# Kernel optimization log

Measured on AMD Instinct MI355X. Metric: run time of the kernel, lower is better.

## Reference

```python
import jax, jax.numpy as jnp
import numpy as np

N = 100000   # nodes
E = 3200000  # edges per graph
DP, DA, DF, H, C = 3, 11, 32, 4, 8  # d_p, d_a, d_feat, heads, per-head dim
NEG_SLOPE = 0.2


def gat_conv(x, edge_index, W, att_src, att_dst, bias):
    """PyG GATConv with concat heads and default add_self_loops=True.
    x: [N, DF]; edge_index: [2, E] (row0=src, row1=dst); W: [DF, H*C];
    att_src/att_dst: [H, C]; bias: [H*C]. Returns [N, H*C]."""
    n = x.shape[0]
    loops = jnp.arange(n, dtype=edge_index.dtype)
    src = jnp.concatenate([edge_index[0], loops])
    dst = jnp.concatenate([edge_index[1], loops])
    h = (x @ W).reshape(n, H, C)                       # [N,H,C]
    a_s = jnp.sum(h * att_src[None], axis=-1)          # [N,H]
    a_d = jnp.sum(h * att_dst[None], axis=-1)          # [N,H]
    e = jax.nn.leaky_relu(a_s[src] + a_d[dst], NEG_SLOPE)  # [Etot,H]
    m = jax.ops.segment_max(e, dst, num_segments=n)        # stable softmax per dst
    ex = jnp.exp(e - m[dst])
    den = jax.ops.segment_sum(ex, dst, num_segments=n)
    alpha = ex / den[dst]                               # [Etot,H]
    out = jax.ops.segment_sum(h[src] * alpha[..., None], dst, num_segments=n)
    return out.reshape(n, H * C) + bias


def setup_inputs() -> dict:
    key = jax.random.key(0)
    ks = jax.random.split(key, 32)
    p = lambda k, shp: (jax.random.normal(k, shp, dtype=jnp.float32) * 0.1)
    inp = {
        "F_p_raw": jax.random.normal(ks[0], (N, DP), dtype=jnp.float32),
        "F_a_raw": jax.random.normal(ks[1], (N, DA), dtype=jnp.float32),
        "edge_index_s": jax.random.randint(ks[2], (2, E), 0, N),
        "edge_index_p": jax.random.randint(ks[3], (2, E), 0, N),
        "edge_index_a": jax.random.randint(ks[4], (2, E), 0, N),
        # align linears
        "Wp": p(ks[5], (DP, DF)), "bp": p(ks[6], (DF,)),
        "Wa": p(ks[7], (DA, DF)), "ba": p(ks[8], (DF,)),
        "Ws": p(ks[9], (DP + DA, DF)), "bs": p(ks[10], (DF,)),
        # GAT params per graph
        "Wg_s": p(ks[11], (DF, H * C)), "asrc_s": p(ks[12], (H, C)), "adst_s": p(ks[13], (H, C)), "bg_s": p(ks[14], (H * C,)),
        "Wg_p": p(ks[15], (DF, H * C)), "asrc_p": p(ks[16], (H, C)), "adst_p": p(ks[17], (H, C)), "bg_p": p(ks[18], (H * C,)),
        "Wg_a": p(ks[19], (DF, H * C)), "asrc_a": p(ks[20], (H, C)), "adst_a": p(ks[21], (H, C)), "bg_a": p(ks[22], (H * C,)),
        # fuse MLP
        "W1": p(ks[23], (3 * DF, DF)), "b1": p(ks[24], (DF,)),
        "W2": p(ks[25], (DF, DF)), "b2": p(ks[26], (DF,)),
    }
    return inp


def reference(F_p_raw, F_a_raw, edge_index_s, edge_index_p, edge_index_a,
              Wp, bp, Wa, ba, Ws, bs,
              Wg_s, asrc_s, adst_s, bg_s,
              Wg_p, asrc_p, adst_p, bg_p,
              Wg_a, asrc_a, adst_a, bg_a,
              W1, b1, W2, b2):
    f_s = jnp.concatenate([F_p_raw, F_a_raw], axis=-1) @ Ws + bs
    f_p = F_p_raw @ Wp + bp
    f_a = F_a_raw @ Wa + ba
    h_s = jax.nn.elu(gat_conv(f_s, edge_index_s, Wg_s, asrc_s, adst_s, bg_s))
    h_p = jax.nn.elu(gat_conv(f_p, edge_index_p, Wg_p, asrc_p, adst_p, bg_p))
    h_a = jax.nn.elu(gat_conv(f_a, edge_index_a, Wg_a, asrc_a, adst_a, bg_a))
    h = jnp.concatenate([h_s, h_p, h_a], axis=-1)
    h = jax.nn.relu(h @ W1 + b1)
    return h @ W2 + b2
```

## Files before the change

### kernel.cpp

```cpp
#include <hip/hip_runtime.h>
#include <hip/hip_bf16.h>
#include <stdint.h>

typedef __hip_bfloat16 bf16;

__device__ __forceinline__ float b2f(bf16 v){ return __bfloat162float(v); }

__device__ __forceinline__ uint16_t f2b(float x){
  uint32_t u = __float_as_uint(x);
  return (uint16_t)((u + 0x7FFFu + ((u >> 16) & 1u)) >> 16);
}

#define DSTS_PER_BKT 128
#define BKT_SHIFT 7
#define CHUNKE 8192
#define CAP 8192
#define PPT 32
#define BIN_IT 32
#define MAXB 1024
#define NBLKMAX 512
#define ROWS_PER_WAVE (DSTS_PER_BKT / 4)

struct CvtTab {
  const void* src[24];
  int n[24];
  int off[24];
};

__global__ __launch_bounds__(256) void k_detect(const void* __restrict__ sample,
                                                int* __restrict__ flag)
{
  __shared__ int bad;
  if (threadIdx.x == 0) bad = 0;
  __syncthreads();
  const unsigned short* u = (const unsigned short*)sample;
  int lbad = 0;
  for (int k = threadIdx.x; k < 1024; k += 256) {
    unsigned short b = u[k];
    unsigned e = (b >> 7) & 0xFFu;
    if (e >= 141u || (e <= 90u && (b & 0x7FFFu) != 0)) lbad = 1;
  }
  if (lbad) atomicOr(&bad, 1);
  __syncthreads();
  if (threadIdx.x == 0) flag[0] = (bad == 0) ? 1 : 0;
}

__global__ __launch_bounds__(256) void k_convert(CvtTab tab, const int* __restrict__ flag,
                                                 float* __restrict__ dst, int total)
{
  const bool isb = (*flag) != 0;
  for (int t = blockIdx.x * 256 + threadIdx.x; t < total; t += gridDim.x * 256) {
    int a = 0;
    while (a < 23 && t >= tab.off[a] + tab.n[a]) ++a;
    int j = t - tab.off[a];
    float v = isb ? b2f(((const bf16*)tab.src[a])[j])
                  : ((const float*)tab.src[a])[j];
    dst[t] = v;
  }
}

__global__ __launch_bounds__(256) void k_node(
  const float* __restrict__ cFp, const float* __restrict__ cFa,
  const float* __restrict__ cWp, const float* __restrict__ cbp,
  const float* __restrict__ cWa, const float* __restrict__ cba,
  const float* __restrict__ cWs, const float* __restrict__ cbs,
  const float* __restrict__ cWg0, const float* __restrict__ cAs0, const float* __restrict__ cAd0,
  const float* __restrict__ cWg1, const float* __restrict__ cAs1, const float* __restrict__ cAd1,
  const float* __restrict__ cWg2, const float* __restrict__ cAs2, const float* __restrict__ cAd2,
  uint32_t* __restrict__ hgb, uint16_t* __restrict__ asb, float* __restrict__ a_d,
  float* __restrict__ den, float* __restrict__ agg, int N)
{
  __shared__ float sWs[14*32];
  __shared__ float sWp[3*32];
  __shared__ float sWa[11*32];
  __shared__ float sb[3][32];
  __shared__ float sWg[3][32*32];
  __shared__ float sA[3][2][32];
  const int tid = threadIdx.x;
  for (int t = tid; t < 14*32; t += 256) sWs[t] = cWs[t];
  for (int t = tid; t < 3*32;  t += 256) sWp[t] = cWp[t];
  for (int t = tid; t < 11*32; t += 256) sWa[t] = cWa[t];
  if (tid < 32) {
    sb[0][tid] = cbs[tid]; sb[1][tid] = cbp[tid]; sb[2][tid] = cba[tid];
    sA[0][0][tid] = cAs0[tid]; sA[0][1][tid] = cAd0[tid];
    sA[1][0][tid] = cAs1[tid]; sA[1][1][tid] = cAd1[tid];
    sA[2][0][tid] = cAs2[tid]; sA[2][1][tid] = cAd2[tid];
  }
  for (int t = tid; t < 32*32; t += 256) {
    sWg[0][t] = cWg0[t]; sWg[1][t] = cWg1[t]; sWg[2][t] = cWg2[t];
  }
  __syncthreads();

  const int i = blockIdx.x * 256 + tid;
  if (i >= N) return;

  float xp[3], xa[11];
  #pragma unroll
  for (int k = 0; k < 3; ++k)  xp[k] = cFp[i*3 + k];
  #pragma unroll
  for (int k = 0; k < 11; ++k) xa[k] = cFa[i*11 + k];

  for (int g = 0; g < 3; ++g) {
    float f[32];
    if (g == 0) {
      #pragma unroll
      for (int j = 0; j < 32; ++j) {
        float acc = sb[0][j];
        #pragma unroll
        for (int k = 0; k < 3; ++k)  acc += xp[k] * sWs[k*32 + j];
        #pragma unroll
        for (int k = 0; k < 11; ++k) acc += xa[k] * sWs[(3+k)*32 + j];
        f[j] = acc;
      }
    } else if (g == 1) {
      #pragma unroll
      for (int j = 0; j < 32; ++j) {
        float acc = sb[1][j];
        #pragma unroll
        for (int k = 0; k < 3; ++k) acc += xp[k] * sWp[k*32 + j];
        f[j] = acc;
      }
    } else {
      #pragma unroll
      for (int j = 0; j < 32; ++j) {
        float acc = sb[2][j];
        #pragma unroll
        for (int k = 0; k < 11; ++k) acc += xa[k] * sWa[k*32 + j];
        f[j] = acc;
      }
    }

    const float* Wg = sWg[g];
    float hv[32];
    #pragma unroll
    for (int j = 0; j < 32; ++j) {
      float acc = 0.f;
      #pragma unroll
      for (int k = 0; k < 32; ++k) acc += f[k] * Wg[k*32 + j];
      hv[j] = acc;
    }

    float asv[4], adv[4], exv[4];
    #pragma unroll
    for (int h = 0; h < 4; ++h) {
      float s0 = 0.f, s1 = 0.f;
      #pragma unroll
      for (int c = 0; c < 8; ++c) {
        s0 += hv[h*8 + c] * sA[g][0][h*8 + c];
        s1 += hv[h*8 + c] * sA[g][1][h*8 + c];
      }
      asv[h] = s0; adv[h] = s1;
      float e = s0 + s1;
      e = e > 0.f ? e : 0.2f * e;
      exv[h] = __expf(e);
    }

    const size_t row = (size_t)g * N + i;
    uint32_t* hp = hgb + row * 16;
    #pragma unroll
    for (int q = 0; q < 4; ++q) {
      uint4 u;
      u.x = (uint32_t)f2b(hv[q*8+0]) | ((uint32_t)f2b(hv[q*8+1]) << 16);
      u.y = (uint32_t)f2b(hv[q*8+2]) | ((uint32_t)f2b(hv[q*8+3]) << 16);
      u.z = (uint32_t)f2b(hv[q*8+4]) | ((uint32_t)f2b(hv[q*8+5]) << 16);
      u.w = (uint32_t)f2b(hv[q*8+6]) | ((uint32_t)f2b(hv[q*8+7]) << 16);
      *(uint4*)(hp + q*4) = u;
    }
    *(ushort4*)(asb + row * 4) =
        make_ushort4(f2b(asv[0]), f2b(asv[1]), f2b(asv[2]), f2b(asv[3]));

    float4* agp = (float4*)(agg + row * 32);
    #pragma unroll
    for (int q = 0; q < 8; ++q) {
      float ex = exv[q >> 1];
      agp[q] = make_float4(ex*hv[q*4+0], ex*hv[q*4+1], ex*hv[q*4+2], ex*hv[q*4+3]);
    }
    *(float4*)(a_d + row*4) = make_float4(adv[0], adv[1], adv[2], adv[3]);
    *(float4*)(den + row*4) = make_float4(exv[0], exv[1], exv[2], exv[3]);
  }
}

__global__ __launch_bounds__(256) void k_bin2(
  const int* __restrict__ ei0, const int* __restrict__ ei1, const int* __restrict__ ei2,
  int* __restrict__ dir, int* __restrict__ bins, int NBPG, int NBLK, int E)
{
  const int g = blockIdx.y;
  const int* __restrict__ ei = (g == 0) ? ei0 : (g == 1 ? ei1 : ei2);
  __shared__ int sp[CHUNKE];
  __shared__ int hist[MAXB];
  __shared__ int soff[MAXB + 1];
  __shared__ int s[256];
  const int tid = threadIdx.x;
  const int blk = blockIdx.x;
  const int base = blk * CHUNKE;
  const int m = min(CHUNKE, E - base);

  for (int t = tid; t < NBPG; t += 256) hist[t] = 0;
  __syncthreads();

  int pk[BIN_IT];
  #pragma unroll
  for (int k = 0; k < BIN_IT; ++k) {
    int idx = base + k * 256 + tid;
    if (idx < E) {
      int d = ei[E + idx];
      int b = d >> BKT_SHIFT;
      int loc = atomicAdd(&hist[b], 1);
      pk[k] = (b << 20) | (loc << 7) | (d & (DSTS_PER_BKT - 1));
    } else pk[k] = -1;
  }
  __syncthreads();

  {
    const int sb = tid * 4;
    int v[4]; int sum = 0;
    #pragma unroll
    for (int j = 0; j < 4; ++j) {
      int i = sb + j; int x = (i < NBPG) ? hist[i] : 0; v[j] = x; sum += x;
    }
    s[tid] = sum;
    __syncthreads();
    for (int d = 1; d < 256; d <<= 1) {
      int t = (tid >= d) ? s[tid - d] : 0;
      __syncthreads();
      s[tid] += t;
      __syncthreads();
    }
    int run = s[tid] - sum;
    #pragma unroll
    for (int j = 0; j < 4; ++j) {
      int i = sb + j;
      if (i < NBPG) { soff[i] = run; run += v[j]; }
    }
    if (tid == 255) soff[NBPG] = s[255];
  }
  __syncthreads();

  for (int t = tid; t <= NBPG; t += 256)
    dir[((size_t)(g * (NBPG + 1) + t)) * NBLK + blk] = soff[t];

  #pragma unroll
  for (int k = 0; k < BIN_IT; ++k) {
    int p = pk[k];
    if (p >= 0) {
      int idx = base + k * 256 + tid;
      int src = ei[idx];
      int b   = p >> 20;
      int loc = (p >> 7) & 0x1FFF;
      int dl  = p & (DSTS_PER_BKT - 1);
      sp[soff[b] + loc] = (dl << 17) | src;
    }
  }
  __syncthreads();

  const size_t ob = ((size_t)(g * NBLK + blk)) << 13;
  for (int i = tid; i < m; i += 256) bins[ob + i] = sp[i];
}

__global__ __launch_bounds__(256, 4) void k_vgather(
  const int* __restrict__ dir, const int* __restrict__ bins,
  const uint32_t* __restrict__ hgb, const uint16_t* __restrict__ asb,
  const float* __restrict__ a_d,
  float* __restrict__ den, float* __restrict__ agg, int NBPG, int NBLK, int N)
{
  __shared__ int sorted[CAP];
  __shared__ int runbase[NBLKMAX];
  __shared__ int pbase[NBLKMAX + 1];
  __shared__ int soff[DSTS_PER_BKT + 1];
  __shared__ int scnt[DSTS_PER_BKT];
  __shared__ int sscan[DSTS_PER_BKT];
  __shared__ int s[256];
  __shared__ int schunk;
  const int g = blockIdx.y, b = blockIdx.x, tid = threadIdx.x;
  const int wave = tid >> 6;
  const int lane = tid & 63;
  const int sub  = lane >> 4;
  const int l16  = lane & 15;
  const int h    = l16 >> 2;
  const int grp16 = tid >> 4;
  const int ln16  = tid & 15;
  const size_t gbase = (size_t)g * N;
  const int dst0 = b * DSTS_PER_BKT;

  const int* d0 = dir + ((size_t)(g * (NBPG + 1) + b)) * NBLK;
  const int* d1 = d0 + NBLK;
  for (int t = tid; t < NBLK; t += 256) {
    int r0 = d0[t], r1 = d1[t];
    runbase[t] = ((g * NBLK + t) << 13) + r0;
    pbase[t] = r1 - r0;
  }
  __syncthreads();
  {
    int v0 = (2*tid     < NBLK) ? pbase[2*tid]     : 0;
    int v1 = (2*tid + 1 < NBLK) ? pbase[2*tid + 1] : 0;
    __syncthreads();
    int sum = v0 + v1; s[tid] = sum;
    __syncthreads();
    for (int d = 1; d < 256; d <<= 1) {
      int t = (tid >= d) ? s[tid - d] : 0;
      __syncthreads();
      s[tid] += t;
      __syncthreads();
    }
    int run = s[tid] - sum;
    if (2*tid     <= NBLK) pbase[2*tid]     = run;
    if (2*tid + 1 <= NBLK) pbase[2*tid + 1] = run + v0;
  }
  __syncthreads();
  const int ntot = pbase[NBLK];

  int rlo = 0;
  while (rlo < NBLK) {
    if (tid == 0) {
      if (rlo == 0 && ntot <= CAP) schunk = NBLK;
      else {
        int lim = pbase[rlo] + CAP;
        int hi = rlo + 1;
        while (hi < NBLK && pbase[hi + 1] <= lim) ++hi;
        schunk = hi;
      }
    }
    if (tid < DSTS_PER_BKT) scnt[tid] = 0;
    __syncthreads();
    const int rhi = schunk;
    const int pb0 = pbase[rlo];
    const int m = pbase[rhi] - pb0;

    for (int rr = rlo + grp16; rr < rhi; rr += 16) {
      const int l = pbase[rr + 1] - pbase[rr];
      const int gbb = runbase[rr];
      const int ldst = pbase[rr] - pb0;
      for (int i = ln16; i < l; i += 16) {
        int p = bins[gbb + i];
        sorted[ldst + i] = p;
        atomicAdd(&scnt[(p >> 17) & (DSTS_PER_BKT - 1)], 1);
      }
    }
    __syncthreads();
    if (tid < DSTS_PER_BKT) sscan[tid] = scnt[tid];
    __syncthreads();
    for (int d = 1; d < DSTS_PER_BKT; d <<= 1) {
      int t = 0;
      if (tid < DSTS_PER_BKT && tid >= d) t = sscan[tid - d];
      __syncthreads();
      if (tid < DSTS_PER_BKT) sscan[tid] += t;
      __syncthreads();
    }
    if (tid < DSTS_PER_BKT) {
      int ex = sscan[tid] - scnt[tid];
      soff[tid] = ex;
      scnt[tid] = ex;
    }
    if (tid == 0) soff[DSTS_PER_BKT] = m;
    __syncthreads();
    int pv[PPT];
    #pragma unroll
    for (int k = 0; k < PPT; ++k) {
      int i = k * 256 + tid;
      pv[k] = (i < m) ? sorted[i] : -1;
    }
    __syncthreads();
    #pragma unroll
    for (int k = 0; k < PPT; ++k) {
      int p = pv[k];
      if (p >= 0) {
        int pos = atomicAdd(&scnt[(p >> 17) & (DSTS_PER_BKT - 1)], 1);
        sorted[pos] = p & 0x1FFFF;
      }
    }
    __syncthreads();

    const int rbeg = wave * ROWS_PER_WAVE;
    for (int rl = rbeg; rl < rbeg + ROWS_PER_WAVE; ++rl) {
      const int dst = dst0 + rl;
      if (dst >= N) break;
      const int cs = soff[rl], ce = soff[rl + 1];
      const size_t row = gbase + dst;
      const float ad = a_d[row * 4 + h];
      float ax = 0.f, ay = 0.f, w = 0.f;
      for (int c = cs + sub; c < ce; c += 16) {
        const int i0 = c        < ce ? sorted[c]      : -1;
        const int i1 = (c + 4)  < ce ? sorted[c + 4]  : -1;
        const int i2 = (c + 8)  < ce ? sorted[c + 8]  : -1;
        const int i3 = (c + 12) < ce ? sorted[c + 12] : -1;
        const int p0 = i0 < 0 ? 0 : i0;
        const int p1 = i1 < 0 ? 0 : i1;
        const int p2 = i2 < 0 ? 0 : i2;
        const int p3 = i3 < 0 ? 0 : i3;
        const uint32_t u0 = hgb[(gbase + p0) * 16 + l16];
        const uint32_t u1 = hgb[(gbase + p1) * 16 + l16];
        const uint32_t u2 = hgb[(gbase + p2) * 16 + l16];
        const uint32_t u3 = hgb[(gbase + p3) * 16 + l16];
        const uint16_t t0 = asb[(gbase + p0) * 4 + h];
        const uint16_t t1 = asb[(gbase + p1) * 4 + h];
        const uint16_t t2 = asb[(gbase + p2) * 4 + h];
        const uint16_t t3 = asb[(gbase + p3) * 4 + h];
        float e0 = __uint_as_float((uint32_t)t0 << 16) + ad; e0 = e0 > 0.f ? e0 : 0.2f * e0;
        float e1 = __uint_as_float((uint32_t)t1 << 16) + ad; e1 = e1 > 0.f ? e1 : 0.2f * e1;
        float e2 = __uint_as_float((uint32_t)t2 << 16) + ad; e2 = e2 > 0.f ? e2 : 0.2f * e2;
        float e3 = __uint_as_float((uint32_t)t3 << 16) + ad; e3 = e3 > 0.f ? e3 : 0.2f * e3;
        const float w0 = i0 >= 0 ? __expf(e0) : 0.f;
        const float w1 = i1 >= 0 ? __expf(e1) : 0.f;
        const float w2 = i2 >= 0 ? __expf(e2) : 0.f;
        const float w3 = i3 >= 0 ? __expf(e3) : 0.f;
        ax += w0 * __uint_as_float(u0 << 16);
        ay += w0 * __uint_as_float(u0 & 0xFFFF0000u);
        ax += w1 * __uint_as_float(u1 << 16);
        ay += w1 * __uint_as_float(u1 & 0xFFFF0000u);
        ax += w2 * __uint_as_float(u2 << 16);
        ay += w2 * __uint_as_float(u2 & 0xFFFF0000u);
        ax += w3 * __uint_as_float(u3 << 16);
        ay += w3 * __uint_as_float(u3 & 0xFFFF0000u);
        w += w0 + w1 + w2 + w3;
      }
      ax += __shfl_xor(ax, 16); ay += __shfl_xor(ay, 16); w += __shfl_xor(w, 16);
      ax += __shfl_xor(ax, 32); ay += __shfl_xor(ay, 32); w += __shfl_xor(w, 32);
      if (sub == 0) {
        float2* ap = (float2*)(agg + row * 32) + l16;
        float2 sv = *ap;
        sv.x += ax; sv.y += ay;
        *ap = sv;
        if ((l16 & 3) == 0) den[row * 4 + h] += w;
      }
    }
    __syncthreads();
    rlo = rhi;
  }
}

__global__ __launch_bounds__(256) void k_final(
  const float* __restrict__ den, const float* __restrict__ agg,
  const float* __restrict__ cbg0, const float* __restrict__ cbg1, const float* __restrict__ cbg2,
  const float* __restrict__ cW1, const float* __restrict__ cb1,
  const float* __restrict__ cW2, const float* __restrict__ cb2,
  const int* __restrict__ flag, void* __restrict__ out, int N)
{
  __shared__ float sW1[96*32];
  __shared__ float sW2[32*32];
  __shared__ float sb1[32], sb2[32], sbg[3][32];
  const int tid = threadIdx.x;
  for (int t = tid; t < 96*32; t += 256) sW1[t] = cW1[t];
  for (int t = tid; t < 32*32; t += 256) sW2[t] = cW2[t];
  if (tid < 32) {
    sb1[tid] = cb1[tid]; sb2[tid] = cb2[tid];
    sbg[0][tid] = cbg0[tid]; sbg[1][tid] = cbg1[tid]; sbg[2][tid] = cbg2[tid];
  }
  __syncthreads();

  const int i = blockIdx.x * 256 + tid;
  if (i >= N) return;

  float h96[96];
  #pragma unroll
  for (int g = 0; g < 3; ++g) {
    const size_t row = (size_t)g * N + i;
    float4 d4 = *(const float4*)(den + row * 4);
    float invs[4] = {1.f/d4.x, 1.f/d4.y, 1.f/d4.z, 1.f/d4.w};
    const float4* av = (const float4*)(agg + row * 32);
    #pragma unroll
    for (int q = 0; q < 8; ++q) {
      float4 a4 = av[q];
      float iv = invs[q >> 1];
      float vals[4] = {a4.x, a4.y, a4.z, a4.w};
      #pragma unroll
      for (int k = 0; k < 4; ++k) {
        float v = vals[k] * iv + sbg[g][q*4 + k];
        v = v > 0.f ? v : (__expf(v) - 1.f);
        h96[g*32 + q*4 + k] = v;
      }
    }
  }

  float h1[32];
  #pragma unroll
  for (int j = 0; j < 32; ++j) {
    float acc = sb1[j];
    #pragma unroll
    for (int k = 0; k < 96; ++k) acc += h96[k] * sW1[k*32 + j];
    h1[j] = acc > 0.f ? acc : 0.f;
  }

  const bool isb = (*flag) != 0;
  #pragma unroll
  for (int j = 0; j < 32; ++j) {
    float acc = sb2[j];
    #pragma unroll
    for (int k = 0; k < 32; ++k) acc += h1[k] * sW2[k*32 + j];
    if (isb) ((bf16*)out)[(size_t)i*32 + j] = __float2bfloat16(acc);
    else     ((float*)out)[(size_t)i*32 + j] = acc;
  }
}

extern "C" void kernel_launch(void* const* d_in, const int* in_sizes, int n_in,
                              void* d_out, int out_size, void* d_ws, size_t ws_size,
                              hipStream_t stream)
{
  const int N = in_sizes[0] / 3;
  const int E = in_sizes[2] / 2;
  const int NBPG = (N + DSTS_PER_BKT - 1) / DSTS_PER_BKT;
  const int NBLK = (E + CHUNKE - 1) / CHUNKE;

  float* ws  = (float*)d_ws;
  int* flag  = (int*)d_ws;
  float* cvt = ws + 64;

  static const int order[24] = {1, 0,
    5, 6, 7, 8, 9, 10,
    11, 12, 13, 14,
    15, 16, 17, 18,
    19, 20, 21, 22,
    23, 24, 25, 26};
  CvtTab tab;
  int off0 = 0;
  for (int a = 0; a < 24; ++a) {
    tab.src[a] = d_in[order[a]];
    tab.n[a]   = in_sizes[order[a]];
    tab.off[a] = off0;
    off0 += tab.n[a];
  }
  const int total = off0;

  float* P[24];
  for (int a = 0; a < 24; ++a) P[a] = cvt + tab.off[a];
  float *cFa = P[0],  *cFp = P[1];
  float *cWp = P[2],  *cbp = P[3],  *cWa = P[4],  *cba = P[5],  *cWs = P[6], *cbs = P[7];
  float *cWg0 = P[8],  *cAs0 = P[9],  *cAd0 = P[10], *cbg0 = P[11];
  float *cWg1 = P[12], *cAs1 = P[13], *cAd1 = P[14], *cbg1 = P[15];
  float *cWg2 = P[16], *cAs2 = P[17], *cAd2 = P[18], *cbg2 = P[19];
  float *cW1 = P[20], *cb1 = P[21], *cW2 = P[22], *cb2 = P[23];

  int pad = (4 - (total & 3)) & 3;
  float* big = cvt + total + pad;
  const size_t n3 = (size_t)3 * N;
  float* agg  = big;
  float* a_d  = agg + n3 * 32;
  float* den  = a_d + n3 * 4;
  uint32_t* hgb = (uint32_t*)(den + n3 * 4);
  uint16_t* asb = (uint16_t*)(hgb + n3 * 16);
  int* dir  = (int*)(asb + n3 * 4);
  int* bins = dir + (size_t)3 * (NBPG + 1) * NBLK;

  k_detect<<<1, 256, 0, stream>>>(d_in[1], flag);
  k_convert<<<2048, 256, 0, stream>>>(tab, flag, cvt, total);
  k_node<<<(N + 255) / 256, 256, 0, stream>>>(
      cFp, cFa, cWp, cbp, cWa, cba, cWs, cbs,
      cWg0, cAs0, cAd0, cWg1, cAs1, cAd1, cWg2, cAs2, cAd2,
      hgb, asb, a_d, den, agg, N);

  dim3 gbk((unsigned)NBLK, 3, 1);
  k_bin2<<<gbk, 256, 0, stream>>>(
      (const int*)d_in[2], (const int*)d_in[3], (const int*)d_in[4],
      dir, bins, NBPG, NBLK, E);

  dim3 gg((unsigned)NBPG, 3, 1);
  k_vgather<<<gg, 256, 0, stream>>>(dir, bins, hgb, asb, a_d, den, agg, NBPG, NBLK, N);

  k_final<<<(N + 255) / 256, 256, 0, stream>>>(
      den, agg, cbg0, cbg1, cbg2, cW1, cb1, cW2, cb2, flag, d_out, N);
}
```

Measured before the change: 432.8 us.

## Drop separate conversion kernel and gather bins with flat binary-searched indexing

```diff
diff --git a/kernel.cpp b/kernel.cpp
--- a/kernel.cpp
+++ b/kernel.cpp
@@ -9,6 +9,10 @@
 __device__ __forceinline__ uint16_t f2b(float x){
   uint32_t u = __float_as_uint(x);
   return (uint16_t)((u + 0x7FFFu + ((u >> 16) & 1u)) >> 16);
+}
+
+__device__ __forceinline__ float loadf(const void* p, int j, bool isb){
+  return isb ? b2f(((const bf16*)p)[j]) : ((const float*)p)[j];
 }
 
 #define DSTS_PER_BKT 128
@@ -21,12 +25,6 @@
 #define NBLKMAX 512
 #define ROWS_PER_WAVE (DSTS_PER_BKT / 4)
 
-struct CvtTab {
-  const void* src[24];
-  int n[24];
-  int off[24];
-};
-
 __global__ __launch_bounds__(256) void k_detect(const void* __restrict__ sample,
                                                 int* __restrict__ flag)
 {
@@ -45,28 +43,15 @@
   if (threadIdx.x == 0) flag[0] = (bad == 0) ? 1 : 0;
 }
 
-__global__ __launch_bounds__(256) void k_convert(CvtTab tab, const int* __restrict__ flag,
-                                                 float* __restrict__ dst, int total)
-{
-  const bool isb = (*flag) != 0;
-  for (int t = blockIdx.x * 256 + threadIdx.x; t < total; t += gridDim.x * 256) {
-    int a = 0;
-    while (a < 23 && t >= tab.off[a] + tab.n[a]) ++a;
-    int j = t - tab.off[a];
-    float v = isb ? b2f(((const bf16*)tab.src[a])[j])
-                  : ((const float*)tab.src[a])[j];
-    dst[t] = v;
-  }
-}
-
 __global__ __launch_bounds__(256) void k_node(
-  const float* __restrict__ cFp, const float* __restrict__ cFa,
-  const float* __restrict__ cWp, const float* __restrict__ cbp,
-  const float* __restrict__ cWa, const float* __restrict__ cba,
-  const float* __restrict__ cWs, const float* __restrict__ cbs,
-  const float* __restrict__ cWg0, const float* __restrict__ cAs0, const float* __restrict__ cAd0,
-  const float* __restrict__ cWg1, const float* __restrict__ cAs1, const float* __restrict__ cAd1,
-  const float* __restrict__ cWg2, const float* __restrict__ cAs2, const float* __restrict__ cAd2,
+  const void* __restrict__ rFp, const void* __restrict__ rFa,
+  const void* __restrict__ rWp, const void* __restrict__ rbp,
+  const void* __restrict__ rWa, const void* __restrict__ rba,
+  const void* __restrict__ rWs, const void* __restrict__ rbs,
+  const void* __restrict__ rWg0, const void* __restrict__ rAs0, const void* __restrict__ rAd0,
+  const void* __restrict__ rWg1, const void* __restrict__ rAs1, const void* __restrict__ rAd1,
+  const void* __restrict__ rWg2, const void* __restrict__ rAs2, const void* __restrict__ rAd2,
+  const int* __restrict__ flag,
   uint32_t* __restrict__ hgb, uint16_t* __restrict__ asb, float* __restrict__ a_d,
   float* __restrict__ den, float* __restrict__ agg, int N)
 {
@@ -77,17 +62,22 @@
   __shared__ float sWg[3][32*32];
   __shared__ float sA[3][2][32];
   const int tid = threadIdx.x;
-  for (int t = tid; t < 14*32; t += 256) sWs[t] = cWs[t];
-  for (int t = tid; t < 3*32;  t += 256) sWp[t] = cWp[t];
-  for (int t = tid; t < 11*32; t += 256) sWa[t] = cWa[t];
+  const bool isb = (*flag) != 0;
+  for (int t = tid; t < 14*32; t += 256) sWs[t] = loadf(rWs, t, isb);
+  for (int t = tid; t < 3*32;  t += 256) sWp[t] = loadf(rWp, t, isb);
+  for (int t = tid; t < 11*32; t += 256) sWa[t] = loadf(rWa, t, isb);
   if (tid < 32) {
-    sb[0][tid] = cbs[tid]; sb[1][tid] = cbp[tid]; sb[2][tid] = cba[tid];
-    sA[0][0][tid] = cAs0[tid]; sA[0][1][tid] = cAd0[tid];
-    sA[1][0][tid] = cAs1[tid]; sA[1][1][tid] = cAd1[tid];
-    sA[2][0][tid] = cAs2[tid]; sA[2][1][tid] = cAd2[tid];
+    sb[0][tid] = loadf(rbs, tid, isb);
+    sb[1][tid] = loadf(rbp, tid, isb);
+    sb[2][tid] = loadf(rba, tid, isb);
+    sA[0][0][tid] = loadf(rAs0, tid, isb); sA[0][1][tid] = loadf(rAd0, tid, isb);
+    sA[1][0][tid] = loadf(rAs1, tid, isb); sA[1][1][tid] = loadf(rAd1, tid, isb);
+    sA[2][0][tid] = loadf(rAs2, tid, isb); sA[2][1][tid] = loadf(rAd2, tid, isb);
   }
   for (int t = tid; t < 32*32; t += 256) {
-    sWg[0][t] = cWg0[t]; sWg[1][t] = cWg1[t]; sWg[2][t] = cWg2[t];
+    sWg[0][t] = loadf(rWg0, t, isb);
+    sWg[1][t] = loadf(rWg1, t, isb);
+    sWg[2][t] = loadf(rWg2, t, isb);
   }
   __syncthreads();
 
@@ -96,9 +86,9 @@
 
   float xp[3], xa[11];
   #pragma unroll
-  for (int k = 0; k < 3; ++k)  xp[k] = cFp[i*3 + k];
-  #pragma unroll
-  for (int k = 0; k < 11; ++k) xa[k] = cFa[i*11 + k];
+  for (int k = 0; k < 3; ++k)  xp[k] = loadf(rFp, i*3 + k, isb);
+  #pragma unroll
+  for (int k = 0; k < 11; ++k) xa[k] = loadf(rFa, i*11 + k, isb);
 
   for (int g = 0; g < 3; ++g) {
     float f[32];
@@ -277,8 +267,6 @@
   const int sub  = lane >> 4;
   const int l16  = lane & 15;
   const int h    = l16 >> 2;
-  const int grp16 = tid >> 4;
-  const int ln16  = tid & 15;
   const size_t gbase = (size_t)g * N;
   const int dst0 = b * DSTS_PER_BKT;
 
@@ -326,13 +314,18 @@
     const int pb0 = pbase[rlo];
     const int m = pbase[rhi] - pb0;
 
-    for (int rr = rlo + grp16; rr < rhi; rr += 16) {
-      const int l = pbase[rr + 1] - pbase[rr];
-      const int gbb = runbase[rr];
-      const int ldst = pbase[rr] - pb0;
-      for (int i = ln16; i < l; i += 16) {
-        int p = bins[gbb + i];
-        sorted[ldst + i] = p;
+    #pragma unroll 4
+    for (int k = 0; k < PPT; ++k) {
+      const int j = k * 256 + tid;
+      if (j < m) {
+        const int j0 = pb0 + j;
+        int lo = rlo, hi = rhi;
+        while (hi - lo > 1) {
+          int mid = (lo + hi) >> 1;
+          if (pbase[mid] <= j0) lo = mid; else hi = mid;
+        }
+        int p = bins[runbase[lo] + (j0 - pbase[lo])];
+        sorted[j] = p;
         atomicAdd(&scnt[(p >> 17) & (DSTS_PER_BKT - 1)], 1);
       }
     }
@@ -430,20 +423,23 @@
 
 __global__ __launch_bounds__(256) void k_final(
   const float* __restrict__ den, const float* __restrict__ agg,
-  const float* __restrict__ cbg0, const float* __restrict__ cbg1, const float* __restrict__ cbg2,
-  const float* __restrict__ cW1, const float* __restrict__ cb1,
-  const float* __restrict__ cW2, const float* __restrict__ cb2,
+  const void* __restrict__ rbg0, const void* __restrict__ rbg1, const void* __restrict__ rbg2,
+  const void* __restrict__ rW1, const void* __restrict__ rb1,
+  const void* __restrict__ rW2, const void* __restrict__ rb2,
   const int* __restrict__ flag, void* __restrict__ out, int N)
 {
   __shared__ float sW1[96*32];
   __shared__ float sW2[32*32];
   __shared__ float sb1[32], sb2[32], sbg[3][32];
   const int tid = threadIdx.x;
-  for (int t = tid; t < 96*32; t += 256) sW1[t] = cW1[t];
-  for (int t = tid; t < 32*32; t += 256) sW2[t] = cW2[t];
+  const bool isb = (*flag) != 0;
+  for (int t = tid; t < 96*32; t += 256) sW1[t] = loadf(rW1, t, isb);
+  for (int t = tid; t < 32*32; t += 256) sW2[t] = loadf(rW2, t, isb);
   if (tid < 32) {
-    sb1[tid] = cb1[tid]; sb2[tid] = cb2[tid];
-    sbg[0][tid] = cbg0[tid]; sbg[1][tid] = cbg1[tid]; sbg[2][tid] = cbg2[tid];
+    sb1[tid] = loadf(rb1, tid, isb); sb2[tid] = loadf(rb2, tid, isb);
+    sbg[0][tid] = loadf(rbg0, tid, isb);
+    sbg[1][tid] = loadf(rbg1, tid, isb);
+    sbg[2][tid] = loadf(rbg2, tid, isb);
   }
   __syncthreads();
 
@@ -480,7 +476,6 @@
     h1[j] = acc > 0.f ? acc : 0.f;
   }
 
-  const bool isb = (*flag) != 0;
   #pragma unroll
   for (int j = 0; j < 32; ++j) {
     float acc = sb2[j];
@@ -500,37 +495,8 @@
   const int NBPG = (N + DSTS_PER_BKT - 1) / DSTS_PER_BKT;
   const int NBLK = (E + CHUNKE - 1) / CHUNKE;
 
-  float* ws  = (float*)d_ws;
-  int* flag  = (int*)d_ws;
-  float* cvt = ws + 64;
-
-  static const int order[24] = {1, 0,
-    5, 6, 7, 8, 9, 10,
-    11, 12, 13, 14,
-    15, 16, 17, 18,
-    19, 20, 21, 22,
-    23, 24, 25, 26};
-  CvtTab tab;
-  int off0 = 0;
-  for (int a = 0; a < 24; ++a) {
-    tab.src[a] = d_in[order[a]];
-    tab.n[a]   = in_sizes[order[a]];
-    tab.off[a] = off0;
-    off0 += tab.n[a];
-  }
-  const int total = off0;
-
-  float* P[24];
-  for (int a = 0; a < 24; ++a) P[a] = cvt + tab.off[a];
-  float *cFa = P[0],  *cFp = P[1];
-  float *cWp = P[2],  *cbp = P[3],  *cWa = P[4],  *cba = P[5],  *cWs = P[6], *cbs = P[7];
-  float *cWg0 = P[8],  *cAs0 = P[9],  *cAd0 = P[10], *cbg0 = P[11];
-  float *cWg1 = P[12], *cAs1 = P[13], *cAd1 = P[14], *cbg1 = P[15];
-  float *cWg2 = P[16], *cAs2 = P[17], *cAd2 = P[18], *cbg2 = P[19];
-  float *cW1 = P[20], *cb1 = P[21], *cW2 = P[22], *cb2 = P[23];
-
-  int pad = (4 - (total & 3)) & 3;
-  float* big = cvt + total + pad;
+  int* flag = (int*)d_ws;
+  float* big = (float*)d_ws + 64;
   const size_t n3 = (size_t)3 * N;
   float* agg  = big;
   float* a_d  = agg + n3 * 32;
@@ -541,11 +507,13 @@
   int* bins = dir + (size_t)3 * (NBPG + 1) * NBLK;
 
   k_detect<<<1, 256, 0, stream>>>(d_in[1], flag);
-  k_convert<<<2048, 256, 0, stream>>>(tab, flag, cvt, total);
   k_node<<<(N + 255) / 256, 256, 0, stream>>>(
-      cFp, cFa, cWp, cbp, cWa, cba, cWs, cbs,
-      cWg0, cAs0, cAd0, cWg1, cAs1, cAd1, cWg2, cAs2, cAd2,
-      hgb, asb, a_d, den, agg, N);
+      d_in[0], d_in[1],
+      d_in[5], d_in[6], d_in[7], d_in[8], d_in[9], d_in[10],
+      d_in[11], d_in[12], d_in[13],
+      d_in[15], d_in[16], d_in[17],
+      d_in[19], d_in[20], d_in[21],
+      flag, hgb, asb, a_d, den, agg, N);
 
   dim3 gbk((unsigned)NBLK, 3, 1);
   k_bin2<<<gbk, 256, 0, stream>>>(
@@ -556,5 +524,6 @@
   k_vgather<<<gg, 256, 0, stream>>>(dir, bins, hgb, asb, a_d, den, agg, NBPG, NBLK, N);
 
   k_final<<<(N + 255) / 256, 256, 0, stream>>>(
-      den, agg, cbg0, cbg1, cbg2, cW1, cb1, cW2, cb2, flag, d_out, N);
-}
+      den, agg, d_in[14], d_in[18], d_in[22],
+      d_in[23], d_in[24], d_in[25], d_in[26], flag, d_out, N);
+}
```

Measured after the change: 455.4 us. +5.2%, slower.
